# Kernel tuning notes

Hardware: AMD Instinct MI355X
Metric: run time of the kernel (lower is better)

Reference implementation:

```python
import jax, jax.numpy as jnp
import numpy as np

M, N, D, K = 32, 8192, 64, 16


def setup_inputs() -> dict:
    key = jax.random.key(0)
    ks = jax.random.split(key, 5)
    X = jax.random.normal(ks[0], (N, D), jnp.float32)
    pi = jax.nn.softmax(jax.random.normal(ks[1], (M,), jnp.float32))  # valid mixture weights
    mu = jax.random.normal(ks[2], (M, D), jnp.float32)
    Lambda_j = 0.1 * jax.random.normal(ks[3], (M, D, K), jnp.float32)  # matches .normal_(0, 0.1) init
    Psi = jax.random.uniform(ks[4], (D,), jnp.float32) + 0.1  # positive diagonal noise variances
    return {"X": X, "pi": pi, "mu": mu, "Lambda_j": Lambda_j, "Psi": Psi}


def _e_step(X, pi, mu, Lambda_j, Psi):
    d = X.shape[1]
    k = Lambda_j.shape[2]
    diag_psi = jnp.diag(Psi) + 1e-6 * jnp.eye(d, dtype=X.dtype)
    # Sigma_j = Lambda_j @ Lambda_j^T + diag(Psi), batched over components: [M,D,D]
    Sigma = jnp.einsum('mdk,mek->mde', Lambda_j, Lambda_j) + diag_psi
    chol = jnp.linalg.cholesky(Sigma)  # [M,D,D], same factorization MultivariateNormal uses
    diff = X[None, :, :] - mu[:, None, :]  # [M,N,D]
    # Mahalanobis term via triangular solve: sol = L^{-1} diff^T  -> [M,D,N]
    sol = jax.vmap(lambda L, Dm: jax.scipy.linalg.solve_triangular(L, Dm.T, lower=True))(chol, diff)
    maha = jnp.sum(sol * sol, axis=1)  # [M,N]
    logdet = 2.0 * jnp.sum(jnp.log(jnp.diagonal(chol, axis1=1, axis2=2)), axis=1)  # [M]
    log_prob = -0.5 * (d * jnp.log(2.0 * jnp.pi) + maha) - 0.5 * logdet[:, None]  # [M,N]
    log_h = (jnp.log(pi + 1e-10)[:, None] + log_prob).T  # [N,M]
    responsibilities = jax.nn.softmax(log_h, axis=1)
    # beta_j = Lambda_j^T Sigma_j^{-1}, via Cholesky solve (same math as torch.inverse path)
    SigInvL = jax.vmap(lambda L, Lam: jax.scipy.linalg.cho_solve((L, True), Lam))(chol, Lambda_j)  # [M,D,K]
    beta = jnp.swapaxes(SigInvL, 1, 2)  # [M,K,D]
    e_z = jnp.einsum('mnd,mkd->mnk', diff, beta)  # [M,N,K]
    term1 = jnp.eye(k, dtype=X.dtype) - jnp.einsum('mkd,mdj->mkj', beta, Lambda_j)  # [M,K,K]
    e_zz = term1[:, None, :, :] + jnp.einsum('mni,mnj->mnij', e_z, e_z)  # [M,N,K,K]
    return responsibilities, e_z, e_zz


def reference(X, pi, mu, Lambda_j, Psi):
    return _e_step(X, pi, mu, Lambda_j, Psi)
```

## Files before the change

### kernel.cpp

```cpp
#include <hip/hip_runtime.h>
#include <math.h>

#define MM 32
#define NN 8192
#define DD 64
#define KK 16

typedef float f32x4 __attribute__((ext_vector_type(4)));

__global__ __launch_bounds__(256) void mfa_pre(
    const float* __restrict__ pi, const float* __restrict__ Lambda,
    const float* __restrict__ Psi, float* __restrict__ Minv_out,
    float* __restrict__ const_out, float* __restrict__ pinv_out,
    float* __restrict__ Wl_out) {
  const int m = blockIdx.x;
  const int tid = threadIdx.x;
  __shared__ float lam[DD * KK];
  __shared__ float pinv[DD];
  __shared__ float Mmat[KK * KK];
  __shared__ float Lmat[KK * KK];
  __shared__ float vbuf[KK];

  for (int idx = tid; idx < DD * KK; idx += 256)
    lam[idx] = Lambda[(size_t)m * DD * KK + idx];
  if (tid < DD) pinv[tid] = 1.0f / (Psi[tid] + 1e-6f);
  __syncthreads();

  for (int idx = tid; idx < DD * KK; idx += 256)
    Wl_out[(size_t)m * DD * KK + idx] = lam[idx] * pinv[idx >> 4];
  if (tid < DD) pinv_out[tid] = pinv[tid];

  {
    const int k = tid >> 4, j = tid & 15;
    float a = 0.0f;
    for (int d = 0; d < DD; ++d)
      a += lam[d * KK + k] * lam[d * KK + j] * pinv[d];
    Mmat[tid] = a + (k == j ? 1.0f : 0.0f);
  }
  __syncthreads();

  float lr[KK];
  if (tid < KK) {
#pragma unroll
    for (int j = 0; j < KK; ++j) lr[j] = Mmat[tid * KK + j];
  }
#pragma unroll
  for (int c = 0; c < KK; ++c) {
    if (tid < KK) vbuf[tid] = lr[c];
    __syncthreads();
    if (tid < KK) {
      const float vc = vbuf[c];
      const float dc = sqrtf(vc);
      const float lrc = lr[c] / dc;
      if (tid >= c) Lmat[tid * KK + c] = lrc;
      const float s = lr[c] / vc;
#pragma unroll
      for (int j = 0; j < KK; ++j)
        if (j > c) lr[j] -= s * vbuf[j];
    }
    __syncthreads();
  }

  if (tid < KK) {
    const int col = tid;
    float y[KK], z[KK];
#pragma unroll
    for (int i = 0; i < KK; ++i) {
      float s = (i == col) ? 1.0f : 0.0f;
#pragma unroll
      for (int p = 0; p < KK; ++p)
        if (p < i) s -= Lmat[i * KK + p] * y[p];
      y[i] = s / Lmat[i * KK + i];
    }
#pragma unroll
    for (int i = KK - 1; i >= 0; --i) {
      float s = y[i];
#pragma unroll
      for (int p = 0; p < KK; ++p)
        if (p > i) s -= Lmat[p * KK + i] * z[p];
      z[i] = s / Lmat[i * KK + i];
    }
#pragma unroll
    for (int i = 0; i < KK; ++i)
      Minv_out[(size_t)m * KK * KK + i * KK + col] = z[i];
  }

  if (tid == 0) {
    float logdetM = 0.0f;
#pragma unroll
    for (int c = 0; c < KK; ++c) logdetM += logf(Lmat[c * KK + c]);
    logdetM *= 2.0f;
    float logdetP = 0.0f;
    for (int d = 0; d < DD; ++d) logdetP -= logf(pinv[d]);
    const float LOG2PI = 1.8378770664093453f;
    const_out[m] =
        logf(pi[m] + 1e-10f) - 0.5f * (DD * LOG2PI + logdetP + logdetM);
  }
}

__global__ __launch_bounds__(256) void mfa_main(
    const float* __restrict__ X, const float* __restrict__ mu,
    const float* __restrict__ Minv, const float* __restrict__ cconst,
    const float* __restrict__ pinvG, const float* __restrict__ WlG,
    float* __restrict__ out) {
  const int m = blockIdx.y;
  const int n0 = blockIdx.x * 256;
  const int tid = threadIdx.x;
  const int w = tid >> 6, l = tid & 63;

  __shared__ float ez_l[256 * KK];

  const float* Wlm = WlG + (size_t)m * DD * KK;
  const float* mum = mu + m * DD;
  const float* Mi = Minv + (size_t)m * KK * KK;
  const float cst = cconst[m];

  const int n = n0 + tid;

  float u[KK];
#pragma unroll
  for (int k = 0; k < KK; ++k) u[k] = 0.0f;
  float q = 0.0f;
  const float4* X4 = reinterpret_cast<const float4*>(X + (size_t)n * DD);
#pragma unroll
  for (int d4 = 0; d4 < DD / 4; ++d4) {
    const float4 xv = X4[d4];
    const float4 muv = *reinterpret_cast<const float4*>(mum + d4 * 4);
    const float4 piv = *reinterpret_cast<const float4*>(pinvG + d4 * 4);
    const float xs[4] = {xv.x, xv.y, xv.z, xv.w};
    const float ms[4] = {muv.x, muv.y, muv.z, muv.w};
    const float ps[4] = {piv.x, piv.y, piv.z, piv.w};
#pragma unroll
    for (int s = 0; s < 4; ++s) {
      const int d = d4 * 4 + s;
      const float df = xs[s] - ms[s];
      q += df * df * ps[s];
      const float4* wr = reinterpret_cast<const float4*>(Wlm + d * KK);
#pragma unroll
      for (int k4 = 0; k4 < 4; ++k4) {
        const float4 wv = wr[k4];
        u[k4 * 4 + 0] += wv.x * df;
        u[k4 * 4 + 1] += wv.y * df;
        u[k4 * 4 + 2] += wv.z * df;
        u[k4 * 4 + 3] += wv.w * df;
      }
    }
  }

  float ez[KK];
  float udot = 0.0f;
#pragma unroll
  for (int i = 0; i < KK; ++i) {
    const float4* mr = reinterpret_cast<const float4*>(Mi + i * KK);
    float s = 0.0f;
#pragma unroll
    for (int j4 = 0; j4 < 4; ++j4) {
      const float4 mv = mr[j4];
      s += mv.x * u[j4 * 4 + 0] + mv.y * u[j4 * 4 + 1] +
           mv.z * u[j4 * 4 + 2] + mv.w * u[j4 * 4 + 3];
    }
    ez[i] = s;
    udot += u[i] * s;
  }
  const float maha = q - udot;
  out[(size_t)n * MM + m] = cst - 0.5f * maha;

#pragma unroll
  for (int k = 0; k < KK; ++k) ez_l[tid * KK + k] = ez[k];

  __builtin_amdgcn_wave_barrier();
  asm volatile("s_waitcnt lgkmcnt(0)" ::: "memory");

  const int sbase = n0 + w * 64;
  const f32x4* ezl4 =
      reinterpret_cast<const f32x4*>(ez_l + (size_t)w * 64 * KK);

  f32x4* ezo = reinterpret_cast<f32x4*>(
      out + (size_t)NN * MM + ((size_t)m * NN + sbase) * KK);
#pragma unroll
  for (int it = 0; it < 4; ++it)
    __builtin_nontemporal_store(ezl4[it * 64 + l], &ezo[it * 64 + l]);

  const int i_ = l >> 2, jq = l & 3;
  const f32x4 mreg = reinterpret_cast<const f32x4*>(Mi)[l];
  f32x4* zzo = reinterpret_cast<f32x4*>(out + (size_t)NN * MM +
                                        (size_t)MM * NN * KK) +
               ((size_t)m * NN + sbase) * 64;
#pragma unroll 4
  for (int nl = 0; nl < 64; ++nl) {
    const float ezi = ez_l[((size_t)w * 64 + nl) * KK + i_];
    const f32x4 ezj = ezl4[nl * 4 + jq];
    const f32x4 o = mreg + ezi * ezj;
    __builtin_nontemporal_store(o, &zzo[nl * 64 + l]);
  }
}

__global__ __launch_bounds__(256) void mfa_softmax(float* __restrict__ out) {
  const int n = blockIdx.x * 256 + threadIdx.x;
  float4* p = reinterpret_cast<float4*>(out) + (size_t)n * (MM / 4);
  float v[MM];
#pragma unroll
  for (int i = 0; i < MM / 4; ++i) {
    const float4 t = p[i];
    v[4 * i] = t.x; v[4 * i + 1] = t.y; v[4 * i + 2] = t.z; v[4 * i + 3] = t.w;
  }
  float mx = -3.4e38f;
#pragma unroll
  for (int i = 0; i < MM; ++i) mx = fmaxf(mx, v[i]);
  float s = 0.0f;
#pragma unroll
  for (int i = 0; i < MM; ++i) { v[i] = expf(v[i] - mx); s += v[i]; }
  const float inv = 1.0f / s;
#pragma unroll
  for (int i = 0; i < MM / 4; ++i) {
    float4 t;
    t.x = v[4 * i] * inv; t.y = v[4 * i + 1] * inv;
    t.z = v[4 * i + 2] * inv; t.w = v[4 * i + 3] * inv;
    p[i] = t;
  }
}

extern "C" void kernel_launch(void* const* d_in, const int* in_sizes, int n_in,
                              void* d_out, int out_size, void* d_ws,
                              size_t ws_size, hipStream_t stream) {
  const float* X = (const float*)d_in[0];
  const float* pi = (const float*)d_in[1];
  const float* mu = (const float*)d_in[2];
  const float* Lambda = (const float*)d_in[3];
  const float* Psi = (const float*)d_in[4];
  float* out = (float*)d_out;

  float* Minv = (float*)d_ws;
  float* cconst = Minv + MM * KK * KK;
  float* pinvG = cconst + MM;
  float* WlG = pinvG + DD;

  mfa_pre<<<MM, 256, 0, stream>>>(pi, Lambda, Psi, Minv, cconst, pinvG, WlG);
  mfa_main<<<dim3(NN / 256, MM), 256, 0, stream>>>(X, mu, Minv, cconst, pinvG,
                                                   WlG, out);
  mfa_softmax<<<NN / 256, 256, 0, stream>>>(out);
}
```

Before: 83.71 us.

## Shrink pre kernel, recompute Psi inverse in main, stage logits in scratch

The precompute kernel now runs one wave per component and no longer writes the scaled Lambda or the inverse Psi to global memory. The main kernel reads Lambda and Psi directly and computes the reciprocal inline. Log-probabilities go to an [M,N] scratch buffer with coalesced writes instead of strided writes into the output. The softmax kernel reads that buffer and writes the final responsibilities. Nontemporal stores for the large e_z and e_zz outputs are replaced with ordinary stores, which may change how the dominant write traffic behaves in cache.

New measurement: 74.00 us, median of 2. 11.6% less time.

```diff
diff --git a/kernel.cpp b/kernel.cpp
--- a/kernel.cpp
+++ b/kernel.cpp
@@ -8,51 +8,55 @@
 
 typedef float f32x4 __attribute__((ext_vector_type(4)));
 
-__global__ __launch_bounds__(256) void mfa_pre(
+__global__ __launch_bounds__(64) void mfa_pre(
     const float* __restrict__ pi, const float* __restrict__ Lambda,
     const float* __restrict__ Psi, float* __restrict__ Minv_out,
-    float* __restrict__ const_out, float* __restrict__ pinv_out,
-    float* __restrict__ Wl_out) {
+    float* __restrict__ const_out) {
   const int m = blockIdx.x;
-  const int tid = threadIdx.x;
+  const int t = threadIdx.x;
   __shared__ float lam[DD * KK];
   __shared__ float pinv[DD];
   __shared__ float Mmat[KK * KK];
   __shared__ float Lmat[KK * KK];
   __shared__ float vbuf[KK];
-
-  for (int idx = tid; idx < DD * KK; idx += 256)
-    lam[idx] = Lambda[(size_t)m * DD * KK + idx];
-  if (tid < DD) pinv[tid] = 1.0f / (Psi[tid] + 1e-6f);
+  __shared__ float red[DD];
+
+  const float4* Lg = reinterpret_cast<const float4*>(Lambda + (size_t)m * DD * KK);
+  float4* lam4 = reinterpret_cast<float4*>(lam);
+  for (int i = t; i < DD * KK / 4; i += 64) lam4[i] = Lg[i];
+  if (t < DD) pinv[t] = 1.0f / (Psi[t] + 1e-6f);
   __syncthreads();
 
-  for (int idx = tid; idx < DD * KK; idx += 256)
-    Wl_out[(size_t)m * DD * KK + idx] = lam[idx] * pinv[idx >> 4];
-  if (tid < DD) pinv_out[tid] = pinv[tid];
-
   {
-    const int k = tid >> 4, j = tid & 15;
-    float a = 0.0f;
-    for (int d = 0; d < DD; ++d)
-      a += lam[d * KK + k] * lam[d * KK + j] * pinv[d];
-    Mmat[tid] = a + (k == j ? 1.0f : 0.0f);
+    const int j = t & 15;
+    const int k0 = t >> 4;
+    float acc[4] = {0.f, 0.f, 0.f, 0.f};
+    for (int d = 0; d < DD; ++d) {
+      const float cj = lam[d * KK + j] * pinv[d];
+#pragma unroll
+      for (int r = 0; r < 4; ++r) acc[r] += lam[d * KK + (k0 + 4 * r)] * cj;
+    }
+#pragma unroll
+    for (int r = 0; r < 4; ++r) {
+      const int k = k0 + 4 * r;
+      Mmat[k * KK + j] = acc[r] + (k == j ? 1.0f : 0.0f);
+    }
   }
   __syncthreads();
 
   float lr[KK];
-  if (tid < KK) {
-#pragma unroll
-    for (int j = 0; j < KK; ++j) lr[j] = Mmat[tid * KK + j];
+  if (t < KK) {
+#pragma unroll
+    for (int j = 0; j < KK; ++j) lr[j] = Mmat[t * KK + j];
   }
 #pragma unroll
   for (int c = 0; c < KK; ++c) {
-    if (tid < KK) vbuf[tid] = lr[c];
+    if (t < KK) vbuf[t] = lr[c];
     __syncthreads();
-    if (tid < KK) {
+    if (t < KK) {
       const float vc = vbuf[c];
       const float dc = sqrtf(vc);
-      const float lrc = lr[c] / dc;
-      if (tid >= c) Lmat[tid * KK + c] = lrc;
+      if (t >= c) Lmat[t * KK + c] = lr[c] / dc;
       const float s = lr[c] / vc;
 #pragma unroll
       for (int j = 0; j < KK; ++j)
@@ -61,8 +65,11 @@
     __syncthreads();
   }
 
-  if (tid < KK) {
-    const int col = tid;
+  if (t < DD) red[t] = logf(pinv[t]);
+  if (t < KK) vbuf[t] = logf(Lmat[t * KK + t]);
+
+  if (t < KK) {
+    const int col = t;
     float y[KK], z[KK];
 #pragma unroll
     for (int i = 0; i < KK; ++i) {
@@ -84,25 +91,25 @@
     for (int i = 0; i < KK; ++i)
       Minv_out[(size_t)m * KK * KK + i * KK + col] = z[i];
   }
-
-  if (tid == 0) {
-    float logdetM = 0.0f;
-#pragma unroll
-    for (int c = 0; c < KK; ++c) logdetM += logf(Lmat[c * KK + c]);
-    logdetM *= 2.0f;
-    float logdetP = 0.0f;
-    for (int d = 0; d < DD; ++d) logdetP -= logf(pinv[d]);
+  __syncthreads();
+
+  if (t == 0) {
+    float sl = 0.0f;
+    for (int d = 0; d < DD; ++d) sl += red[d];
+    float lM = 0.0f;
+#pragma unroll
+    for (int c = 0; c < KK; ++c) lM += vbuf[c];
     const float LOG2PI = 1.8378770664093453f;
     const_out[m] =
-        logf(pi[m] + 1e-10f) - 0.5f * (DD * LOG2PI + logdetP + logdetM);
+        logf(pi[m] + 1e-10f) - 0.5f * (DD * LOG2PI - sl + 2.0f * lM);
   }
 }
 
 __global__ __launch_bounds__(256) void mfa_main(
     const float* __restrict__ X, const float* __restrict__ mu,
+    const float* __restrict__ Lambda, const float* __restrict__ Psi,
     const float* __restrict__ Minv, const float* __restrict__ cconst,
-    const float* __restrict__ pinvG, const float* __restrict__ WlG,
-    float* __restrict__ out) {
+    float* __restrict__ scr, float* __restrict__ out) {
   const int m = blockIdx.y;
   const int n0 = blockIdx.x * 256;
   const int tid = threadIdx.x;
@@ -110,7 +117,7 @@
 
   __shared__ float ez_l[256 * KK];
 
-  const float* Wlm = WlG + (size_t)m * DD * KK;
+  const float* lamG = Lambda + (size_t)m * DD * KK;
   const float* mum = mu + m * DD;
   const float* Mi = Minv + (size_t)m * KK * KK;
   const float cst = cconst[m];
@@ -126,47 +133,50 @@
   for (int d4 = 0; d4 < DD / 4; ++d4) {
     const float4 xv = X4[d4];
     const float4 muv = *reinterpret_cast<const float4*>(mum + d4 * 4);
-    const float4 piv = *reinterpret_cast<const float4*>(pinvG + d4 * 4);
+    const float4 psv = *reinterpret_cast<const float4*>(Psi + d4 * 4);
     const float xs[4] = {xv.x, xv.y, xv.z, xv.w};
     const float ms[4] = {muv.x, muv.y, muv.z, muv.w};
-    const float ps[4] = {piv.x, piv.y, piv.z, piv.w};
+    const float ps[4] = {psv.x, psv.y, psv.z, psv.w};
 #pragma unroll
     for (int s = 0; s < 4; ++s) {
       const int d = d4 * 4 + s;
       const float df = xs[s] - ms[s];
-      q += df * df * ps[s];
-      const float4* wr = reinterpret_cast<const float4*>(Wlm + d * KK);
+      const float dfp = df * __builtin_amdgcn_rcpf(ps[s] + 1e-6f);
+      q += df * dfp;
+      const float4* wr = reinterpret_cast<const float4*>(lamG + d * KK);
 #pragma unroll
       for (int k4 = 0; k4 < 4; ++k4) {
         const float4 wv = wr[k4];
-        u[k4 * 4 + 0] += wv.x * df;
-        u[k4 * 4 + 1] += wv.y * df;
-        u[k4 * 4 + 2] += wv.z * df;
-        u[k4 * 4 + 3] += wv.w * df;
+        u[k4 * 4 + 0] += wv.x * dfp;
+        u[k4 * 4 + 1] += wv.y * dfp;
+        u[k4 * 4 + 2] += wv.z * dfp;
+        u[k4 * 4 + 3] += wv.w * dfp;
       }
     }
   }
 
-  float ez[KK];
   float udot = 0.0f;
-#pragma unroll
-  for (int i = 0; i < KK; ++i) {
-    const float4* mr = reinterpret_cast<const float4*>(Mi + i * KK);
-    float s = 0.0f;
-#pragma unroll
-    for (int j4 = 0; j4 < 4; ++j4) {
-      const float4 mv = mr[j4];
-      s += mv.x * u[j4 * 4 + 0] + mv.y * u[j4 * 4 + 1] +
-           mv.z * u[j4 * 4 + 2] + mv.w * u[j4 * 4 + 3];
-    }
-    ez[i] = s;
-    udot += u[i] * s;
-  }
-  const float maha = q - udot;
-  out[(size_t)n * MM + m] = cst - 0.5f * maha;
-
-#pragma unroll
-  for (int k = 0; k < KK; ++k) ez_l[tid * KK + k] = ez[k];
+  float* ezrow = ez_l + (size_t)tid * KK;
+#pragma unroll
+  for (int i4 = 0; i4 < 4; ++i4) {
+    f32x4 ezv;
+#pragma unroll
+    for (int ii = 0; ii < 4; ++ii) {
+      const int i = i4 * 4 + ii;
+      const float4* mr = reinterpret_cast<const float4*>(Mi + i * KK);
+      float s = 0.0f;
+#pragma unroll
+      for (int j4 = 0; j4 < 4; ++j4) {
+        const float4 mv = mr[j4];
+        s += mv.x * u[j4 * 4 + 0] + mv.y * u[j4 * 4 + 1] +
+             mv.z * u[j4 * 4 + 2] + mv.w * u[j4 * 4 + 3];
+      }
+      ezv[ii] = s;
+      udot += u[i] * s;
+    }
+    *reinterpret_cast<f32x4*>(ezrow + i4 * 4) = ezv;
+  }
+  scr[(size_t)m * NN + n] = cst - 0.5f * (q - udot);
 
   __builtin_amdgcn_wave_barrier();
   asm volatile("s_waitcnt lgkmcnt(0)" ::: "memory");
@@ -178,8 +188,7 @@
   f32x4* ezo = reinterpret_cast<f32x4*>(
       out + (size_t)NN * MM + ((size_t)m * NN + sbase) * KK);
 #pragma unroll
-  for (int it = 0; it < 4; ++it)
-    __builtin_nontemporal_store(ezl4[it * 64 + l], &ezo[it * 64 + l]);
+  for (int it = 0; it < 4; ++it) ezo[it * 64 + l] = ezl4[it * 64 + l];
 
   const int i_ = l >> 2, jq = l & 3;
   const f32x4 mreg = reinterpret_cast<const f32x4*>(Mi)[l];
@@ -190,20 +199,16 @@
   for (int nl = 0; nl < 64; ++nl) {
     const float ezi = ez_l[((size_t)w * 64 + nl) * KK + i_];
     const f32x4 ezj = ezl4[nl * 4 + jq];
-    const f32x4 o = mreg + ezi * ezj;
-    __builtin_nontemporal_store(o, &zzo[nl * 64 + l]);
-  }
-}
-
-__global__ __launch_bounds__(256) void mfa_softmax(float* __restrict__ out) {
-  const int n = blockIdx.x * 256 + threadIdx.x;
-  float4* p = reinterpret_cast<float4*>(out) + (size_t)n * (MM / 4);
+    zzo[nl * 64 + l] = mreg + ezi * ezj;
+  }
+}
+
+__global__ __launch_bounds__(64) void mfa_softmax(
+    const float* __restrict__ scr, float* __restrict__ out) {
+  const int n = blockIdx.x * 64 + threadIdx.x;
   float v[MM];
 #pragma unroll
-  for (int i = 0; i < MM / 4; ++i) {
-    const float4 t = p[i];
-    v[4 * i] = t.x; v[4 * i + 1] = t.y; v[4 * i + 2] = t.z; v[4 * i + 3] = t.w;
-  }
+  for (int m = 0; m < MM; ++m) v[m] = scr[(size_t)m * NN + n];
   float mx = -3.4e38f;
 #pragma unroll
   for (int i = 0; i < MM; ++i) mx = fmaxf(mx, v[i]);
@@ -211,6 +216,7 @@
 #pragma unroll
   for (int i = 0; i < MM; ++i) { v[i] = expf(v[i] - mx); s += v[i]; }
   const float inv = 1.0f / s;
+  float4* p = reinterpret_cast<float4*>(out) + (size_t)n * (MM / 4);
 #pragma unroll
   for (int i = 0; i < MM / 4; ++i) {
     float4 t;
@@ -232,11 +238,10 @@
 
   float* Minv = (float*)d_ws;
   float* cconst = Minv + MM * KK * KK;
-  float* pinvG = cconst + MM;
-  float* WlG = pinvG + DD;
-
-  mfa_pre<<<MM, 256, 0, stream>>>(pi, Lambda, Psi, Minv, cconst, pinvG, WlG);
-  mfa_main<<<dim3(NN / 256, MM), 256, 0, stream>>>(X, mu, Minv, cconst, pinvG,
-                                                   WlG, out);
-  mfa_softmax<<<NN / 256, 256, 0, stream>>>(out);
-}
+  float* scr = cconst + MM;
+
+  mfa_pre<<<MM, 64, 0, stream>>>(pi, Lambda, Psi, Minv, cconst);
+  mfa_main<<<dim3(NN / 256, MM), 256, 0, stream>>>(X, mu, Lambda, Psi, Minv,
+                                                   cconst, scr, out);
+  mfa_softmax<<<NN / 64, 64, 0, stream>>>(scr, out);
+}
```
